# Optimization experiments

Measured on AMD Instinct MI355X. Metric: run time of the kernel, lower is better.

The kernel has to match this reference:

```python
import jax, jax.numpy as jnp
import numpy as np

N = 200000   # nodes
E = 400000   # edges
G = 4096     # graphs in batch
F_IN = 77    # atom feature dim
D = 128      # dim_drug
L = 3        # layer_drug
BN_EPS = 1e-5


def setup_inputs() -> dict:
    key = jax.random.key(0)
    ks = jax.random.split(key, 16)
    inp = {}
    inp["x"] = jax.random.normal(ks[0], (N, F_IN), jnp.float32)
    inp["edge_index"] = jax.random.randint(ks[1], (2, E), 0, N, dtype=jnp.int64)
    inp["batch"] = jnp.sort(jax.random.randint(ks[2], (N,), 0, G, dtype=jnp.int64))
    dims = [F_IN, D, D]
    i = 3
    for l in range(L):
        din = dims[l]
        inp[f"w1_{l}"] = jax.random.normal(ks[i], (din, D), jnp.float32) / np.sqrt(din); i += 1
        inp[f"b1_{l}"] = jnp.zeros((D,), jnp.float32)
        inp[f"w2_{l}"] = jax.random.normal(ks[i], (D, D), jnp.float32) / np.sqrt(D); i += 1
        inp[f"b2_{l}"] = jnp.zeros((D,), jnp.float32)
        inp[f"gamma_{l}"] = jnp.ones((D,), jnp.float32)
        inp[f"beta_{l}"] = jnp.zeros((D,), jnp.float32)
    inp["w_emb"] = jax.random.normal(ks[i], (L * D, 256), jnp.float32) / np.sqrt(L * D)
    inp["b_emb"] = jnp.zeros((256,), jnp.float32)
    return inp


def _gin_bn_layer(h, src, dst, w1, b1, w2, b2, gamma, beta):
    # GINConv (eps=0): out_i = MLP(x_i + sum_{j->i} x_j)
    agg = jax.ops.segment_sum(h[src], dst, num_segments=N)  # scatter-add aggregation
    h = h + agg
    h = jax.nn.relu(h @ w1 + b1) @ w2 + b2                  # GIN MLP
    h = jax.nn.relu(h)                                       # outer F.relu
    mu = jnp.mean(h, axis=0)
    var = jnp.var(h, axis=0)                                  # biased var (training-mode BN)
    return (h - mu) * jax.lax.rsqrt(var + BN_EPS) * gamma + beta


def reference(x, edge_index, batch,
              w1_0, b1_0, w2_0, b2_0, gamma_0, beta_0,
              w1_1, b1_1, w2_1, b2_1, gamma_1, beta_1,
              w1_2, b1_2, w2_2, b2_2, gamma_2, beta_2,
              w_emb, b_emb):
    src, dst = edge_index[0], edge_index[1]
    layers = [(w1_0, b1_0, w2_0, b2_0, gamma_0, beta_0),
              (w1_1, b1_1, w2_1, b2_1, gamma_1, beta_1),
              (w1_2, b1_2, w2_2, b2_2, gamma_2, beta_2)]
    h = x
    outs = []
    for (w1, b1, w2, b2, g, b) in layers:
        h = _gin_bn_layer(h, src, dst, w1, b1, w2, b2, g, b)
        outs.append(h)
    node_rep = jnp.concatenate(outs, axis=1)                  # JK 'cat' -> [N, L*D]
    pooled = jax.ops.segment_max(node_rep, batch, num_segments=G)  # global_max_pool -> [G, L*D]
    # drug_emb: Linear -> ReLU -> Dropout (identity in eval)
    return jax.nn.relu(pooled @ w_emb + b_emb)
```

## Files before the change

### kernel.cpp

```cpp
#include <hip/hip_runtime.h>
#include <hip/hip_bf16.h>
#include <float.h>

#define NN 200000
#define NE 400000
#define NG 4096
#define FIN 77
#define DD 128
#define BN_EPS 1e-5f
#define NB_SCAN ((NN + 255) / 256)
#define NBLK (NN / 64)

typedef float f32x4 __attribute__((ext_vector_type(4)));
typedef short s16x8 __attribute__((ext_vector_type(8)));

__device__ __forceinline__ unsigned short f2bf(float x) {
    unsigned b = __float_as_uint(x);
    unsigned r = (b + 0x7FFFu + ((b >> 16) & 1u)) >> 16;
    return (unsigned short)r;
}
__device__ __forceinline__ float bf2f(unsigned short u) {
    return __uint_as_float(((unsigned)u) << 16);
}

__global__ void detect_kernel(const unsigned* eidx, const unsigned* batch, int* flags) {
    if (threadIdx.x == 0 && blockIdx.x == 0) {
        int e64 = 1, b64 = 1;
        for (int i = 0; i < 16; i++) {
            if (eidx[2 * NE - 1 - 2 * i] != 0u) e64 = 0;
            if (batch[NN - 1 - 2 * i] != 0u) b64 = 0;
        }
        flags[0] = e64;
        flags[1] = b64;
    }
}

__device__ __forceinline__ int load_idx(const void* p, int is64, long long i) {
    return is64 ? (int)((const long long*)p)[i] : ((const int*)p)[i];
}

__global__ void graph_starts_kernel(const void* batch, const int* flags, int* start) {
    int g = blockIdx.x * blockDim.x + threadIdx.x;
    if (g > NG) return;
    int is64 = flags[1];
    int lo = 0, hi = NN;
    while (lo < hi) {
        int mid = (lo + hi) >> 1;
        int v = load_idx(batch, is64, mid);
        if (v < g) lo = mid + 1; else hi = mid;
    }
    start[g] = lo;
}

__global__ void count_kernel(const void* __restrict__ eidx, const int* __restrict__ flags,
                             int* __restrict__ deg) {
    int e = blockIdx.x * 256 + threadIdx.x;
    if (e >= NE) return;
    int dst = load_idx(eidx, flags[0], (long long)NE + e);
    atomicAdd(&deg[dst], 1);
}

__global__ void scan1_kernel(const int* __restrict__ deg, int* __restrict__ incl,
                             int* __restrict__ bsum) {
    __shared__ int sh[256];
    int i = blockIdx.x * 256 + threadIdx.x;
    int v = (i < NN) ? deg[i] : 0;
    sh[threadIdx.x] = v;
    __syncthreads();
    for (int off = 1; off < 256; off <<= 1) {
        int t = (threadIdx.x >= off) ? sh[threadIdx.x - off] : 0;
        __syncthreads();
        sh[threadIdx.x] += t;
        __syncthreads();
    }
    if (i < NN) incl[i] = sh[threadIdx.x];
    if (threadIdx.x == 255) bsum[blockIdx.x] = sh[255];
}

__global__ void scan2_kernel(int* __restrict__ bsum) {
    __shared__ int sh[NB_SCAN];
    for (int i = threadIdx.x; i < NB_SCAN; i += blockDim.x) sh[i] = bsum[i];
    __syncthreads();
    if (threadIdx.x == 0) {
        int acc = 0;
        for (int i = 0; i < NB_SCAN; i++) { int t = sh[i]; sh[i] = acc; acc += t; }
    }
    __syncthreads();
    for (int i = threadIdx.x; i < NB_SCAN; i += blockDim.x) bsum[i] = sh[i];
}

__global__ void scan3_kernel(const int* __restrict__ incl, const int* __restrict__ deg,
                             const int* __restrict__ bsum, int* __restrict__ rowptr,
                             int* __restrict__ cursor) {
    int i = blockIdx.x * 256 + threadIdx.x;
    if (i < NN) {
        int ex = bsum[blockIdx.x] + incl[i] - deg[i];
        rowptr[i] = ex;
        cursor[i] = ex;
    }
    if (i == 0) rowptr[NN] = NE;
}

__global__ void fill_kernel(const void* __restrict__ eidx, const int* __restrict__ flags,
                            int* __restrict__ cursor, int* __restrict__ slots) {
    int e = blockIdx.x * 256 + threadIdx.x;
    if (e >= NE) return;
    int is64 = flags[0];
    int src = load_idx(eidx, is64, e);
    int dst = load_idx(eidx, is64, (long long)NE + e);
    int pos = atomicAdd(&cursor[dst], 1);
    slots[pos] = src;
}

__global__ void meta_kernel(const int* __restrict__ rowptr, const int* __restrict__ slots,
                            int4* __restrict__ meta) {
    int i = blockIdx.x * 256 + threadIdx.x;
    if (i >= NN) return;
    int lo = rowptr[i], hi = rowptr[i + 1];
    int d = hi - lo;
    int s0 = (d > 0) ? slots[lo] : i;
    int s1 = (d > 1) ? slots[lo + 1] : i;
    meta[i] = make_int4(s0, s1, d, lo);
}

__global__ void xconv_kernel(const float* __restrict__ x, unsigned short* __restrict__ xb) {
    int idx = blockIdx.x * 256 + threadIdx.x;
    int row = idx / 12, c8 = (idx % 12) * 8;
    union { s16x8 v; unsigned short u[8]; } pk;
#pragma unroll
    for (int j = 0; j < 8; j++) {
        int c = c8 + j;
        pk.u[j] = (c < FIN) ? f2bf(x[(long long)row * FIN + c]) : (unsigned short)0;
    }
    *(s16x8*)&xb[(long long)row * 96 + c8] = pk.v;
}

__global__ void wconv_kernel(const float* __restrict__ w1, const float* __restrict__ w2,
                             unsigned short* __restrict__ wt1, unsigned short* __restrict__ wt2,
                             int K1) {
    int idx = blockIdx.x * 256 + threadIdx.x;
    int c = idx >> 7, k = idx & 127;
    wt1[idx] = f2bf(k < K1 ? w1[k * DD + c] : 0.f);
    wt2[idx] = f2bf(w2[k * DD + c]);
}

template <int L0>
__global__ __launch_bounds__(256) void fused_layer(
    const unsigned short* __restrict__ src, const float* __restrict__ ss,
    const int4* __restrict__ meta, const int* __restrict__ slots,
    const unsigned short* __restrict__ wt1, const unsigned short* __restrict__ wt2,
    const float* __restrict__ b1, const float* __restrict__ b2,
    unsigned short* __restrict__ out, float* __restrict__ partials)
{
    __shared__ unsigned short Xs[64 * 128];
    constexpr int SK = L0 ? 96 : 128;
    constexpr int KS1 = L0 ? 3 : 4;
    int tid = threadIdx.x;
    int lane = tid & 63;
    int w = tid >> 6;
    long long rowBase = (long long)blockIdx.x * 64;

    {
        int rp = tid >> 4;
        int c8 = (tid & 15) * 8;
        float sc[8], sh[8];
        if (!L0) {
#pragma unroll
            for (int j = 0; j < 8; j++) { sc[j] = ss[c8 + j]; sh[j] = ss[DD + c8 + j]; }
        }
#pragma unroll
        for (int p = 0; p < 4; p++) {
            int r = p * 16 + rp;
            long long gr = rowBase + r;
            float a[8];
            if (L0 && c8 >= 96) {
#pragma unroll
                for (int j = 0; j < 8; j++) a[j] = 0.f;
            } else {
                int4 mt = meta[gr];
                long long s0 = mt.x, s1 = mt.y;
                int d = mt.z, lo = mt.w;
                s16x8 vo = *(const s16x8*)&src[gr * SK + c8];
                s16x8 v0 = *(const s16x8*)&src[s0 * SK + c8];
                s16x8 v1 = *(const s16x8*)&src[s1 * SK + c8];
                float m0 = (d > 0) ? 1.f : 0.f, m1 = (d > 1) ? 1.f : 0.f;
#pragma unroll
                for (int j = 0; j < 8; j++)
                    a[j] = bf2f((unsigned short)vo[j]) + m0 * bf2f((unsigned short)v0[j])
                                                      + m1 * bf2f((unsigned short)v1[j]);
                for (int k = 2; k < d; k++) {
                    long long sk = slots[lo + k];
                    s16x8 vk = *(const s16x8*)&src[sk * SK + c8];
#pragma unroll
                    for (int j = 0; j < 8; j++) a[j] += bf2f((unsigned short)vk[j]);
                }
                if (!L0) {
                    float cnt = (float)(d + 1);
#pragma unroll
                    for (int j = 0; j < 8; j++) a[j] = a[j] * sc[j] + cnt * sh[j];
                }
            }
            union { s16x8 v; unsigned short u[8]; } pk;
#pragma unroll
            for (int j = 0; j < 8; j++) pk.u[j] = f2bf(a[j]);
            *(s16x8*)&Xs[r * 128 + (c8 ^ ((r & 7) << 3))] = pk.v;
        }
    }

    int colbase = w * 32 + (lane & 15);
    s16x8 w1f[2][4], w2f[2][4];
#pragma unroll
    for (int cb = 0; cb < 2; cb++) {
        int col = colbase + cb * 16;
#pragma unroll
        for (int ks = 0; ks < KS1; ks++)
            w1f[cb][ks] = *(const s16x8*)&wt1[col * 128 + ks * 32 + (lane >> 4) * 8];
#pragma unroll
        for (int ks = 0; ks < 4; ks++)
            w2f[cb][ks] = *(const s16x8*)&wt2[col * 128 + ks * 32 + (lane >> 4) * 8];
    }
    float bs1[2], bs2[2];
#pragma unroll
    for (int cb = 0; cb < 2; cb++) {
        bs1[cb] = b1[colbase + cb * 16];
        bs2[cb] = b2[colbase + cb * 16];
    }

    __syncthreads();

    f32x4 acc[4][2];
#pragma unroll
    for (int rb = 0; rb < 4; rb++)
#pragma unroll
        for (int cb = 0; cb < 2; cb++) acc[rb][cb] = 0;
#pragma unroll
    for (int ks = 0; ks < KS1; ks++) {
        int lk = ks * 32 + (lane >> 4) * 8;
        s16x8 af[4];
#pragma unroll
        for (int rb = 0; rb < 4; rb++) {
            int r = rb * 16 + (lane & 15);
            af[rb] = *(const s16x8*)&Xs[r * 128 + (lk ^ ((r & 7) << 3))];
        }
#pragma unroll
        for (int rb = 0; rb < 4; rb++)
#pragma unroll
            for (int cb = 0; cb < 2; cb++)
                acc[rb][cb] = __builtin_amdgcn_mfma_f32_16x16x32_bf16(af[rb], w1f[cb][ks], acc[rb][cb], 0, 0, 0);
    }

    __syncthreads();

#pragma unroll
    for (int rb = 0; rb < 4; rb++)
#pragma unroll
        for (int cb = 0; cb < 2; cb++) {
            int col = colbase + cb * 16;
#pragma unroll
            for (int reg = 0; reg < 4; reg++) {
                int row = rb * 16 + (lane >> 4) * 4 + reg;
                float v = fmaxf(acc[rb][cb][reg] + bs1[cb], 0.f);
                Xs[row * 128 + (col ^ ((row & 7) << 3))] = f2bf(v);
            }
        }

    __syncthreads();

#pragma unroll
    for (int rb = 0; rb < 4; rb++)
#pragma unroll
        for (int cb = 0; cb < 2; cb++) acc[rb][cb] = 0;
#pragma unroll
    for (int ks = 0; ks < 4; ks++) {
        int lk = ks * 32 + (lane >> 4) * 8;
        s16x8 af[4];
#pragma unroll
        for (int rb = 0; rb < 4; rb++) {
            int r = rb * 16 + (lane & 15);
            af[rb] = *(const s16x8*)&Xs[r * 128 + (lk ^ ((r & 7) << 3))];
        }
#pragma unroll
        for (int rb = 0; rb < 4; rb++)
#pragma unroll
            for (int cb = 0; cb < 2; cb++)
                acc[rb][cb] = __builtin_amdgcn_mfma_f32_16x16x32_bf16(af[rb], w2f[cb][ks], acc[rb][cb], 0, 0, 0);
    }

    float ps[2] = {0.f, 0.f}, pq[2] = {0.f, 0.f};
#pragma unroll
    for (int rb = 0; rb < 4; rb++)
#pragma unroll
        for (int cb = 0; cb < 2; cb++) {
            int col = colbase + cb * 16;
#pragma unroll
            for (int reg = 0; reg < 4; reg++) {
                long long row = rowBase + rb * 16 + (lane >> 4) * 4 + reg;
                float v = fmaxf(acc[rb][cb][reg] + bs2[cb], 0.f);
                unsigned short ub = f2bf(v);
                out[row * DD + col] = ub;
                float vb = bf2f(ub);
                ps[cb] += vb;
                pq[cb] += vb * vb;
            }
        }
#pragma unroll
    for (int cb = 0; cb < 2; cb++) {
        ps[cb] += __shfl_xor(ps[cb], 16); ps[cb] += __shfl_xor(ps[cb], 32);
        pq[cb] += __shfl_xor(pq[cb], 16); pq[cb] += __shfl_xor(pq[cb], 32);
        if (lane < 16) {
            int col = colbase + cb * 16;
            partials[(long long)blockIdx.x * 256 + col] = ps[cb];
            partials[(long long)blockIdx.x * 256 + 128 + col] = pq[cb];
        }
    }
}

__global__ void bn_red2_kernel(const float* __restrict__ partials, float* __restrict__ sums) {
    float s = 0.f;
    for (int b = blockIdx.x; b < NBLK; b += gridDim.x)
        s += partials[(long long)b * 256 + threadIdx.x];
    atomicAdd(&sums[threadIdx.x], s);
}

__global__ void bn_finalize_kernel(const float* __restrict__ sums,
                                   const float* __restrict__ gamma,
                                   const float* __restrict__ beta,
                                   float* __restrict__ ss) {
    int c = threadIdx.x;
    float mu = sums[c] / (float)NN;
    float var = sums[DD + c] / (float)NN - mu * mu;
    float sc = gamma[c] * rsqrtf(var + BN_EPS);
    ss[c] = sc;
    ss[DD + c] = beta[c] - mu * sc;
}

__global__ __launch_bounds__(256) void pool_kernel(const unsigned short* __restrict__ hm,
                                                   const float* __restrict__ ss,
                                                   const int* __restrict__ start,
                                                   float* __restrict__ pooled, int l) {
    __shared__ float red[256];
    int g = blockIdx.x;
    int c = threadIdx.x & 127;
    int half = threadIdx.x >> 7;
    int lo = start[g], hi = start[g + 1];
    float sc = ss[c], sh = ss[DD + c];
    float m = -FLT_MAX;
    for (int n = lo + half; n < hi; n += 2)
        m = fmaxf(m, bf2f(hm[(long long)n * DD + c]) * sc + sh);
    red[threadIdx.x] = m;
    __syncthreads();
    if (threadIdx.x < 128)
        pooled[(long long)g * (3 * DD) + l * DD + c] = fmaxf(red[threadIdx.x], red[threadIdx.x + 128]);
}

__global__ __launch_bounds__(256) void emb_kernel(const float* __restrict__ pooled,
                                                  const float* __restrict__ w,
                                                  const float* __restrict__ b,
                                                  float* __restrict__ out) {
    __shared__ float pl[8][384];
    int tid = threadIdx.x;
    int g0 = blockIdx.x * 8;
#pragma unroll
    for (int i = 0; i < 12; i++) {
        int idx = tid + i * 256;
        int gg = idx / 384, c = idx % 384;
        pl[gg][c] = pooled[(long long)(g0 + gg) * 384 + c];
    }
    __syncthreads();
    float acc[8];
#pragma unroll
    for (int gg = 0; gg < 8; gg++) acc[gg] = 0.f;
    for (int k = 0; k < 384; k++) {
        float wv = w[k * 256 + tid];
#pragma unroll
        for (int gg = 0; gg < 8; gg++) acc[gg] += pl[gg][k] * wv;
    }
    float bb = b[tid];
#pragma unroll
    for (int gg = 0; gg < 8; gg++)
        out[(long long)(g0 + gg) * 256 + tid] = fmaxf(acc[gg] + bb, 0.f);
}

extern "C" void kernel_launch(void* const* d_in, const int* in_sizes, int n_in,
                              void* d_out, int out_size, void* d_ws, size_t ws_size,
                              hipStream_t stream) {
    const float* x = (const float*)d_in[0];
    const void* eidx = d_in[1];
    const void* batch = d_in[2];
    const float* w1[3] = { (const float*)d_in[3],  (const float*)d_in[9],  (const float*)d_in[15] };
    const float* b1[3] = { (const float*)d_in[4],  (const float*)d_in[10], (const float*)d_in[16] };
    const float* w2[3] = { (const float*)d_in[5],  (const float*)d_in[11], (const float*)d_in[17] };
    const float* b2[3] = { (const float*)d_in[6],  (const float*)d_in[12], (const float*)d_in[18] };
    const float* gm[3] = { (const float*)d_in[7],  (const float*)d_in[13], (const float*)d_in[19] };
    const float* bt[3] = { (const float*)d_in[8],  (const float*)d_in[14], (const float*)d_in[20] };
    const float* w_emb = (const float*)d_in[21];
    const float* b_emb = (const float*)d_in[22];
    float* out = (float*)d_out;

    unsigned short* R1 = (unsigned short*)d_ws;
    unsigned short* R2 = R1 + (size_t)NN * DD;
    float* pooled = (float*)(R2 + (size_t)NN * DD);
    float* partials = pooled + (size_t)NG * 384;
    unsigned short* wtb = (unsigned short*)(partials + (size_t)NBLK * 256);
    float* sums = (float*)(wtb + 6 * 16384);
    float* ss = sums + 256;
    int* start = (int*)(ss + 256);
    int* flags = start + NG + 1;
    int* deg = flags + 3;
    int* incl = deg + NN;
    int* bsum = incl + NN;
    int* rowptr = bsum + NB_SCAN;
    int* cursor = rowptr + NN + 1;
    int* slots = cursor + NN;
    int4* meta = (int4*)(((size_t)(slots + NE) + 15) & ~(size_t)15);

    detect_kernel<<<1, 64, 0, stream>>>((const unsigned*)eidx, (const unsigned*)batch, flags);
    graph_starts_kernel<<<(NG + 1 + 255) / 256, 256, 0, stream>>>(batch, flags, start);

    hipMemsetAsync(deg, 0, (size_t)NN * sizeof(int), stream);
    count_kernel<<<(NE + 255) / 256, 256, 0, stream>>>(eidx, flags, deg);
    scan1_kernel<<<NB_SCAN, 256, 0, stream>>>(deg, incl, bsum);
    scan2_kernel<<<1, 1024, 0, stream>>>(bsum);
    scan3_kernel<<<NB_SCAN, 256, 0, stream>>>(incl, deg, bsum, rowptr, cursor);
    fill_kernel<<<(NE + 255) / 256, 256, 0, stream>>>(eidx, flags, cursor, slots);
    meta_kernel<<<NB_SCAN, 256, 0, stream>>>(rowptr, slots, meta);

    xconv_kernel<<<(NN * 12) / 256, 256, 0, stream>>>(x, R1);
    for (int l = 0; l < 3; l++)
        wconv_kernel<<<64, 256, 0, stream>>>(w1[l], w2[l], wtb + l * 2 * 16384,
                                             wtb + l * 2 * 16384 + 16384, (l == 0) ? FIN : DD);

    unsigned short* hin[3] = { R1, R2, R1 };
    unsigned short* hout[3] = { R2, R1, R2 };
    for (int l = 0; l < 3; l++) {
        const unsigned short* wt1 = wtb + l * 2 * 16384;
        const unsigned short* wt2 = wt1 + 16384;
        hipMemsetAsync(sums, 0, 256 * sizeof(float), stream);
        if (l == 0)
            fused_layer<1><<<NBLK, 256, 0, stream>>>(hin[l], ss, meta, slots, wt1, wt2,
                                                     b1[l], b2[l], hout[l], partials);
        else
            fused_layer<0><<<NBLK, 256, 0, stream>>>(hin[l], ss, meta, slots, wt1, wt2,
                                                     b1[l], b2[l], hout[l], partials);
        bn_red2_kernel<<<256, 256, 0, stream>>>(partials, sums);
        bn_finalize_kernel<<<1, 128, 0, stream>>>(sums, gm[l], bt[l], ss);
        pool_kernel<<<NG, 256, 0, stream>>>(hout[l], ss, start, pooled, l);
    }
    emb_kernel<<<NG / 8, 256, 0, stream>>>(pooled, w_emb, b_emb, out);
}
```

Baseline: 426.7 us.

## Cut kernel launches: fuse BN finalize, merge weight conversion, drop meta kernel

```diff
diff --git a/kernel.cpp b/kernel.cpp
--- a/kernel.cpp
+++ b/kernel.cpp
@@ -78,15 +78,18 @@
 }
 
 __global__ void scan2_kernel(int* __restrict__ bsum) {
-    __shared__ int sh[NB_SCAN];
-    for (int i = threadIdx.x; i < NB_SCAN; i += blockDim.x) sh[i] = bsum[i];
-    __syncthreads();
-    if (threadIdx.x == 0) {
-        int acc = 0;
-        for (int i = 0; i < NB_SCAN; i++) { int t = sh[i]; sh[i] = acc; acc += t; }
-    }
-    __syncthreads();
-    for (int i = threadIdx.x; i < NB_SCAN; i += blockDim.x) bsum[i] = sh[i];
+    __shared__ int sh[1024];
+    int t = threadIdx.x;
+    int orig = (t < NB_SCAN) ? bsum[t] : 0;
+    sh[t] = orig;
+    __syncthreads();
+    for (int off = 1; off < 1024; off <<= 1) {
+        int v = (t >= off) ? sh[t - off] : 0;
+        __syncthreads();
+        sh[t] += v;
+        __syncthreads();
+    }
+    if (t < NB_SCAN) bsum[t] = sh[t] - orig;
 }
 
 __global__ void scan3_kernel(const int* __restrict__ incl, const int* __restrict__ deg,
@@ -112,17 +115,6 @@
     slots[pos] = src;
 }
 
-__global__ void meta_kernel(const int* __restrict__ rowptr, const int* __restrict__ slots,
-                            int4* __restrict__ meta) {
-    int i = blockIdx.x * 256 + threadIdx.x;
-    if (i >= NN) return;
-    int lo = rowptr[i], hi = rowptr[i + 1];
-    int d = hi - lo;
-    int s0 = (d > 0) ? slots[lo] : i;
-    int s1 = (d > 1) ? slots[lo + 1] : i;
-    meta[i] = make_int4(s0, s1, d, lo);
-}
-
 __global__ void xconv_kernel(const float* __restrict__ x, unsigned short* __restrict__ xb) {
     int idx = blockIdx.x * 256 + threadIdx.x;
     int row = idx / 12, c8 = (idx % 12) * 8;
@@ -135,19 +127,25 @@
     *(s16x8*)&xb[(long long)row * 96 + c8] = pk.v;
 }
 
-__global__ void wconv_kernel(const float* __restrict__ w1, const float* __restrict__ w2,
-                             unsigned short* __restrict__ wt1, unsigned short* __restrict__ wt2,
-                             int K1) {
-    int idx = blockIdx.x * 256 + threadIdx.x;
+__global__ void wconv_all_kernel(const float* __restrict__ w10, const float* __restrict__ w20,
+                                 const float* __restrict__ w11, const float* __restrict__ w21,
+                                 const float* __restrict__ w12, const float* __restrict__ w22,
+                                 unsigned short* __restrict__ wtb) {
+    int l = blockIdx.x >> 6;
+    int idx = (blockIdx.x & 63) * 256 + threadIdx.x;
     int c = idx >> 7, k = idx & 127;
+    const float* w1 = (l == 0) ? w10 : ((l == 1) ? w11 : w12);
+    const float* w2 = (l == 0) ? w20 : ((l == 1) ? w21 : w22);
+    int K1 = (l == 0) ? FIN : DD;
+    unsigned short* wt1 = wtb + l * 2 * 16384;
     wt1[idx] = f2bf(k < K1 ? w1[k * DD + c] : 0.f);
-    wt2[idx] = f2bf(w2[k * DD + c]);
+    wt1[16384 + idx] = f2bf(w2[k * DD + c]);
 }
 
 template <int L0>
 __global__ __launch_bounds__(256) void fused_layer(
     const unsigned short* __restrict__ src, const float* __restrict__ ss,
-    const int4* __restrict__ meta, const int* __restrict__ slots,
+    const int* __restrict__ rowptr, const int* __restrict__ slots,
     const unsigned short* __restrict__ wt1, const unsigned short* __restrict__ wt2,
     const float* __restrict__ b1, const float* __restrict__ b2,
     unsigned short* __restrict__ out, float* __restrict__ partials)
@@ -177,9 +175,10 @@
 #pragma unroll
                 for (int j = 0; j < 8; j++) a[j] = 0.f;
             } else {
-                int4 mt = meta[gr];
-                long long s0 = mt.x, s1 = mt.y;
-                int d = mt.z, lo = mt.w;
+                int lo = rowptr[gr], hi = rowptr[gr + 1];
+                int d = hi - lo;
+                long long s0 = (d > 0) ? (long long)slots[lo] : gr;
+                long long s1 = (d > 1) ? (long long)slots[lo + 1] : gr;
                 s16x8 vo = *(const s16x8*)&src[gr * SK + c8];
                 s16x8 v0 = *(const s16x8*)&src[s0 * SK + c8];
                 s16x8 v1 = *(const s16x8*)&src[s1 * SK + c8];
@@ -188,8 +187,8 @@
                 for (int j = 0; j < 8; j++)
                     a[j] = bf2f((unsigned short)vo[j]) + m0 * bf2f((unsigned short)v0[j])
                                                       + m1 * bf2f((unsigned short)v1[j]);
-                for (int k = 2; k < d; k++) {
-                    long long sk = slots[lo + k];
+                for (int k = lo + 2; k < hi; k++) {
+                    long long sk = slots[k];
                     s16x8 vk = *(const s16x8*)&src[sk * SK + c8];
 #pragma unroll
                     for (int j = 0; j < 8; j++) a[j] += bf2f((unsigned short)vk[j]);
@@ -315,23 +314,28 @@
     }
 }
 
-__global__ void bn_red2_kernel(const float* __restrict__ partials, float* __restrict__ sums) {
+__global__ __launch_bounds__(256) void bn_red2_fin_kernel(
+    const float* __restrict__ partials, float* __restrict__ sums, int* __restrict__ done,
+    const float* __restrict__ gamma, const float* __restrict__ beta, float* __restrict__ ss) {
     float s = 0.f;
     for (int b = blockIdx.x; b < NBLK; b += gridDim.x)
         s += partials[(long long)b * 256 + threadIdx.x];
     atomicAdd(&sums[threadIdx.x], s);
-}
-
-__global__ void bn_finalize_kernel(const float* __restrict__ sums,
-                                   const float* __restrict__ gamma,
-                                   const float* __restrict__ beta,
-                                   float* __restrict__ ss) {
-    int c = threadIdx.x;
-    float mu = sums[c] / (float)NN;
-    float var = sums[DD + c] / (float)NN - mu * mu;
-    float sc = gamma[c] * rsqrtf(var + BN_EPS);
-    ss[c] = sc;
-    ss[DD + c] = beta[c] - mu * sc;
+    __threadfence();
+    __syncthreads();
+    __shared__ int tick;
+    if (threadIdx.x == 0) tick = atomicAdd(done, 1);
+    __syncthreads();
+    if (tick == (int)gridDim.x - 1 && threadIdx.x < 128) {
+        int c = threadIdx.x;
+        float s0 = atomicAdd(&sums[c], 0.f);
+        float s1 = atomicAdd(&sums[DD + c], 0.f);
+        float mu = s0 / (float)NN;
+        float var = s1 / (float)NN - mu * mu;
+        float sc = gamma[c] * rsqrtf(var + BN_EPS);
+        ss[c] = sc;
+        ss[DD + c] = beta[c] - mu * sc;
+    }
 }
 
 __global__ __launch_bounds__(256) void pool_kernel(const unsigned short* __restrict__ hm,
@@ -344,10 +348,17 @@
     int half = threadIdx.x >> 7;
     int lo = start[g], hi = start[g + 1];
     float sc = ss[c], sh = ss[DD + c];
-    float m = -FLT_MAX;
-    for (int n = lo + half; n < hi; n += 2)
-        m = fmaxf(m, bf2f(hm[(long long)n * DD + c]) * sc + sh);
-    red[threadIdx.x] = m;
+    float m0 = -FLT_MAX, m1 = -FLT_MAX;
+    int n = lo + half;
+    for (; n + 2 < hi; n += 4) {
+        float v0 = bf2f(hm[(long long)n * DD + c]) * sc + sh;
+        float v1 = bf2f(hm[(long long)(n + 2) * DD + c]) * sc + sh;
+        m0 = fmaxf(m0, v0);
+        m1 = fmaxf(m1, v1);
+    }
+    for (; n < hi; n += 2)
+        m0 = fmaxf(m0, bf2f(hm[(long long)n * DD + c]) * sc + sh);
+    red[threadIdx.x] = fmaxf(m0, m1);
     __syncthreads();
     if (threadIdx.x < 128)
         pooled[(long long)g * (3 * DD) + l * DD + c] = fmaxf(red[threadIdx.x], red[threadIdx.x + 128]);
@@ -402,49 +413,49 @@
     float* pooled = (float*)(R2 + (size_t)NN * DD);
     float* partials = pooled + (size_t)NG * 384;
     unsigned short* wtb = (unsigned short*)(partials + (size_t)NBLK * 256);
-    float* sums = (float*)(wtb + 6 * 16384);
-    float* ss = sums + 256;
-    int* start = (int*)(ss + 256);
-    int* flags = start + NG + 1;
-    int* deg = flags + 3;
+    float* ss = (float*)(wtb + 6 * 16384);
+    float* sums = ss + 3 * 256;
+    int* done = (int*)(sums + 3 * 256);
+    int* deg = done + 4;
+    size_t zbytes = (3 * 256) * sizeof(float) + 4 * sizeof(int) + (size_t)NN * sizeof(int);
     int* incl = deg + NN;
     int* bsum = incl + NN;
     int* rowptr = bsum + NB_SCAN;
     int* cursor = rowptr + NN + 1;
     int* slots = cursor + NN;
-    int4* meta = (int4*)(((size_t)(slots + NE) + 15) & ~(size_t)15);
+    int* start = slots + NE;
+    int* flags = start + NG + 1;
 
     detect_kernel<<<1, 64, 0, stream>>>((const unsigned*)eidx, (const unsigned*)batch, flags);
     graph_starts_kernel<<<(NG + 1 + 255) / 256, 256, 0, stream>>>(batch, flags, start);
 
-    hipMemsetAsync(deg, 0, (size_t)NN * sizeof(int), stream);
+    hipMemsetAsync(sums, 0, zbytes, stream);
+
     count_kernel<<<(NE + 255) / 256, 256, 0, stream>>>(eidx, flags, deg);
     scan1_kernel<<<NB_SCAN, 256, 0, stream>>>(deg, incl, bsum);
     scan2_kernel<<<1, 1024, 0, stream>>>(bsum);
     scan3_kernel<<<NB_SCAN, 256, 0, stream>>>(incl, deg, bsum, rowptr, cursor);
     fill_kernel<<<(NE + 255) / 256, 256, 0, stream>>>(eidx, flags, cursor, slots);
-    meta_kernel<<<NB_SCAN, 256, 0, stream>>>(rowptr, slots, meta);
 
     xconv_kernel<<<(NN * 12) / 256, 256, 0, stream>>>(x, R1);
-    for (int l = 0; l < 3; l++)
-        wconv_kernel<<<64, 256, 0, stream>>>(w1[l], w2[l], wtb + l * 2 * 16384,
-                                             wtb + l * 2 * 16384 + 16384, (l == 0) ? FIN : DD);
+    wconv_all_kernel<<<192, 256, 0, stream>>>(w1[0], w2[0], w1[1], w2[1], w1[2], w2[2], wtb);
 
     unsigned short* hin[3] = { R1, R2, R1 };
     unsigned short* hout[3] = { R2, R1, R2 };
     for (int l = 0; l < 3; l++) {
         const unsigned short* wt1 = wtb + l * 2 * 16384;
         const unsigned short* wt2 = wt1 + 16384;
-        hipMemsetAsync(sums, 0, 256 * sizeof(float), stream);
+        const float* ss_prev = ss + (l - 1) * 256;
+        float* ss_l = ss + l * 256;
         if (l == 0)
-            fused_layer<1><<<NBLK, 256, 0, stream>>>(hin[l], ss, meta, slots, wt1, wt2,
+            fused_layer<1><<<NBLK, 256, 0, stream>>>(hin[l], nullptr, rowptr, slots, wt1, wt2,
                                                      b1[l], b2[l], hout[l], partials);
         else
-            fused_layer<0><<<NBLK, 256, 0, stream>>>(hin[l], ss, meta, slots, wt1, wt2,
+            fused_layer<0><<<NBLK, 256, 0, stream>>>(hin[l], ss_prev, rowptr, slots, wt1, wt2,
                                                      b1[l], b2[l], hout[l], partials);
-        bn_red2_kernel<<<256, 256, 0, stream>>>(partials, sums);
-        bn_finalize_kernel<<<1, 128, 0, stream>>>(sums, gm[l], bt[l], ss);
-        pool_kernel<<<NG, 256, 0, stream>>>(hout[l], ss, start, pooled, l);
+        bn_red2_fin_kernel<<<256, 256, 0, stream>>>(partials, sums + l * 256, done + l,
+                                                    gm[l], bt[l], ss_l);
+        pool_kernel<<<NG, 256, 0, stream>>>(hout[l], ss_l, start, pooled, l);
     }
     emb_kernel<<<NG / 8, 256, 0, stream>>>(pooled, w_emb, b_emb, out);
 }
```

New measurement: 460.8 us. +8.0%, slower.
